# Kernel tuning notes

Measured on AMD Instinct MI355X. Metric: run time of the kernel, lower is better.

## Reference

```python
import jax, jax.numpy as jnp
import numpy as np

N, E, G = 20000, 640000, 64
D_IN, H, C, D_OUT = 256, 4, 64, 32
HC = H * C


def gat_layer(x, W, a_src, a_dst, b, src, dst, n_nodes, heads, ch):
    # x: [N, F_in], W: [F_in, H*C]
    h = (x @ W).reshape(n_nodes, heads, ch)          # [N,H,C]
    es = jnp.einsum('nhc,hc->nh', h, a_src)          # [N,H]
    ed = jnp.einsum('nhc,hc->nh', h, a_dst)
    e = jax.nn.leaky_relu(es[src] + ed[dst], 0.2)    # [Etot,H]
    m = jax.ops.segment_max(e, dst, num_segments=n_nodes)
    m = jnp.where(jnp.isfinite(m), m, 0.0)
    ex = jnp.exp(e - m[dst])
    denom = jax.ops.segment_sum(ex, dst, num_segments=n_nodes)
    alpha = ex / jnp.maximum(denom[dst], 1e-16)      # softmax over in-edges per dst
    out = jax.ops.segment_sum(alpha[:, :, None] * h[src], dst, num_segments=n_nodes)
    return out.reshape(n_nodes, heads * ch) + b


def setup_inputs() -> dict:
    key = jax.random.key(0)
    ks = jax.random.split(key, 14)
    g1 = 1.0 / np.sqrt(D_IN)
    g2 = 1.0 / np.sqrt(HC)
    inp = {
        'x': jax.random.normal(ks[0], (N, D_IN), jnp.float32),
        'edge_index': jax.random.randint(ks[1], (2, E), 0, N, jnp.int64 if jax.config.jax_enable_x64 else jnp.int32),
        'batch': jnp.sort(jax.random.randint(ks[2], (N,), 0, G)),
        'W1': jax.random.normal(ks[3], (D_IN, HC), jnp.float32) * g1,
        'a_src1': jax.random.normal(ks[4], (H, C), jnp.float32) * g2,
        'a_dst1': jax.random.normal(ks[5], (H, C), jnp.float32) * g2,
        'b1': jnp.zeros((HC,), jnp.float32),
        'W2': jax.random.normal(ks[6], (HC, HC), jnp.float32) * g2,
        'a_src2': jax.random.normal(ks[7], (H, C), jnp.float32) * g2,
        'a_dst2': jax.random.normal(ks[8], (H, C), jnp.float32) * g2,
        'b2': jnp.zeros((HC,), jnp.float32),
        'Wp': jax.random.normal(ks[9], (HC, D_OUT), jnp.float32) * g2,
        'bp': jnp.zeros((D_OUT,), jnp.float32),
    }
    return inp


def reference(x, edge_index, batch, W1, a_src1, a_dst1, b1, W2, a_src2, a_dst2, b2, Wp, bp):
    # add self-loops (PyG GATConv default)
    loop = jnp.arange(N, dtype=edge_index.dtype)
    src = jnp.concatenate([edge_index[0], loop])
    dst = jnp.concatenate([edge_index[1], loop])
    x1 = jax.nn.relu(gat_layer(x, W1, a_src1, a_dst1, b1, src, dst, N, H, C))
    # dropout p=0.6 is identity in eval mode
    x2 = jax.nn.relu(gat_layer(x1, W2, a_src2, a_dst2, b2, src, dst, N, H, C))
    node_scores = x2 @ Wp + bp                        # [N, D_OUT]
    sums = jax.ops.segment_sum(node_scores, batch, num_segments=G)
    counts = jax.ops.segment_sum(jnp.ones((N,), node_scores.dtype), batch, num_segments=G)
    return sums / jnp.maximum(counts, 1.0)[:, None]   # [G, D_OUT]
```

## Files before the change

kernel.cpp:

```cpp
#include <hip/hip_runtime.h>
#include <hip/hip_bf16.h>
#include <cstdint>

#define NNODES 20000
#define NEDGES 640000
#define ETOT   (NEDGES + NNODES)
#define NGROUP 64
#define HC     256
#define DOUT   32
#define EBLK   5120
#define NBLK   (NEDGES / EBLK)
#define CBLK   ((NNODES + 255) / 256)
#define GBLK   (NNODES / 16)
#define HALFN  10240

typedef short bf16x8 __attribute__((ext_vector_type(8)));
typedef short s16x4  __attribute__((ext_vector_type(4)));
typedef float f32x4  __attribute__((ext_vector_type(4)));
typedef float f32x2  __attribute__((ext_vector_type(2)));
typedef int   s32x4  __attribute__((ext_vector_type(4)));
typedef unsigned int u32x4 __attribute__((ext_vector_type(4)));

__device__ __forceinline__ float bs2f(short v) {
    union { unsigned int u; float f; } c; c.u = ((unsigned int)(unsigned short)v) << 16; return c.f;
}
__device__ __forceinline__ short f2bs(float v) {
    __hip_bfloat16 b = __float2bfloat16(v);
    union { __hip_bfloat16 b; short s; } u; u.b = b; return u.s;
}
__device__ __forceinline__ float ldf(const void* __restrict__ p, size_t i, int bf) {
    return bf ? __bfloat162float(((const __hip_bfloat16*)p)[i]) : ((const float*)p)[i];
}
__device__ __forceinline__ int ld_idx(const int* __restrict__ p, size_t i, int f64) {
    return f64 ? p[2 * i] : p[i];
}
__device__ __forceinline__ unsigned enc_f(float f) {
    unsigned u = __float_as_uint(f);
    return (u >> 31) ? ~u : (u | 0x80000000u);
}
__device__ __forceinline__ float dec_f(unsigned e) {
    return (e >> 31) ? __uint_as_float(e & 0x7FFFFFFFu) : __uint_as_float(~e);
}
__device__ __forceinline__ int probe_edge64(const int* __restrict__ ei) {
    int l = threadIdx.x & 63;
    int zeros = 0;
#pragma unroll
    for (int r = 0; r < 4; r++)
        zeros += __popcll(__ballot(ei[2 * (r * 64 + l) + 1] == 0));
    return (zeros > 200) ? 1 : 0;
}
__device__ __forceinline__ int probe_xbf(const unsigned int* __restrict__ xw) {
    int l = threadIdx.x & 63;
    int ones = 0;
#pragma unroll
    for (int r = 0; r < 4; r++)
        ones += __popcll(__ballot((xw[r * 64 + l] >> 14) & 1));
    return (ones < 64) ? 1 : 0;
}

__global__ __launch_bounds__(256) void k_setup(const unsigned int* __restrict__ xw,
                                               const int* __restrict__ ei,
                                               const int* __restrict__ bat,
                                               const void* __restrict__ W1, const void* __restrict__ W2,
                                               __hip_bfloat16* __restrict__ Wt1,
                                               __hip_bfloat16* __restrict__ Wt2,
                                               int* __restrict__ H,
                                               float* __restrict__ sx, int* __restrict__ cnt,
                                               unsigned* __restrict__ gp2) {
    __shared__ int hl[NNODES];
    int t = threadIdx.x, b = blockIdx.x;
    if (b < NBLK) {
        int f = probe_edge64(ei);
        s32x4* hl4 = reinterpret_cast<s32x4*>(hl);
        for (int i = t; i < NNODES / 4; i += 256) hl4[i] = (s32x4){0, 0, 0, 0};
        __syncthreads();
        int s0 = b * EBLK;
        if (f) {
            const int* d64 = ei + 2 * NEDGES;
            for (int i0 = s0; i0 < s0 + EBLK; i0 += 512) {
                int i = i0 + 2 * t;
                s32x4 v = *reinterpret_cast<const s32x4*>(d64 + 2 * (size_t)i);
                atomicAdd(&hl[v[0]], 1);
                atomicAdd(&hl[v[2]], 1);
            }
        } else {
            const int* d32 = ei + NEDGES;
            for (int i0 = s0; i0 < s0 + EBLK; i0 += 1024) {
                int i = i0 + 4 * t;
                s32x4 v = *reinterpret_cast<const s32x4*>(d32 + i);
                atomicAdd(&hl[v[0]], 1); atomicAdd(&hl[v[1]], 1);
                atomicAdd(&hl[v[2]], 1); atomicAdd(&hl[v[3]], 1);
            }
        }
        __syncthreads();
        s32x4* Hb4 = reinterpret_cast<s32x4*>(H + (size_t)b * NNODES);
        for (int i = t; i < NNODES / 4; i += 256) Hb4[i] = hl4[i];
    } else {
        int bf = probe_xbf(xw);
        int i = (b - NBLK) * 256 + t;
        int which = i >> 16;
        int j = i & 65535;
        int k = j >> 8, n = j & 255;
        const void* W = which ? W2 : W1;
        __hip_bfloat16* Wt = which ? Wt2 : Wt1;
        Wt[(size_t)n * 256 + k] = __float2bfloat16(ldf(W, (size_t)k * 256 + n, bf));
        if (b == NBLK) {
            for (int q = t; q < NGROUP * HC; q += 256) sx[q] = 0.f;
            if (t < 256) gp2[t] = 0x007FFFFFu;
            int f = probe_edge64(ei);
            if (t < NGROUP) hl[t] = 0;
            __syncthreads();
            for (int r = t; r < NNODES; r += 256) atomicAdd(&hl[ld_idx(bat, r, f)], 1);
            __syncthreads();
            if (t < NGROUP) cnt[t] = hl[t];
        }
    }
}

__global__ __launch_bounds__(256) void k_colsum(const int* __restrict__ H,
                                                int* __restrict__ deg,
                                                int* __restrict__ bsum) {
    __shared__ int wred[4];
    int t = threadIdx.x, n = blockIdx.x * 256 + t;
    int s = 0;
    if (n < NNODES) {
#pragma unroll 5
        for (int b = 0; b < NBLK; b++) s += H[(size_t)b * NNODES + n];
        s += 1;
        deg[n] = s;
    }
    int r = s;
#pragma unroll
    for (int o = 1; o < 64; o <<= 1) r += __shfl_xor(r, o);
    if ((t & 63) == 0) wred[t >> 6] = r;
    __syncthreads();
    if (t == 0) bsum[blockIdx.x] = wred[0] + wred[1] + wred[2] + wred[3];
}

__global__ __launch_bounds__(256) void k_base(int* __restrict__ H,
                                              const int* __restrict__ deg,
                                              const int* __restrict__ bsum,
                                              int* __restrict__ off,
                                              int* __restrict__ csr) {
    __shared__ int wtot[4];
    __shared__ int boff_s;
    int t = threadIdx.x, blk = blockIdx.x;
    int n = blk * 256 + t;
    int d = (n < NNODES) ? deg[n] : 0;
    int lane = t & 63, w = t >> 6;
    int sc = d;
#pragma unroll
    for (int o = 1; o < 64; o <<= 1) {
        int u = __shfl_up(sc, o);
        if (lane >= o) sc += u;
    }
    if (lane == 63) wtot[w] = sc;
    if (w == 0) {
        int v = (lane < blk) ? bsum[lane] : 0;
        if (lane + 64 < blk) v += bsum[lane + 64];
#pragma unroll
        for (int o = 1; o < 64; o <<= 1) v += __shfl_xor(v, o);
        if (lane == 0) boff_s = v;
    }
    __syncthreads();
    int woff = 0;
    for (int i = 0; i < w; i++) woff += wtot[i];
    int excl = woff + sc - d;
    if (blk == 0 && t == 0) off[NNODES] = ETOT;
    if (n < NNODES) {
        int o0 = boff_s + excl;
        off[n] = o0;
        csr[o0] = n;
        int run = o0 + 1;
#pragma unroll 5
        for (int b = 0; b < NBLK; b++) {
            size_t idx = (size_t)b * NNODES + n;
            int tt = H[idx];
            H[idx] = run;
            run += tt;
        }
    }
}

__device__ __forceinline__ void dev_scatter(int b, int f, const int* __restrict__ ei,
                                            const int* __restrict__ H, int* __restrict__ csr,
                                            int* hl) {
    int t = threadIdx.x;
    for (int pass = 0; pass < 2; ++pass) {
        int nbase = pass * HALFN;
        int span = NNODES - nbase; if (span > HALFN) span = HALFN;
        const int* Hb = H + (size_t)b * NNODES + nbase;
        for (int i = t; i < span; i += 256) hl[i] = Hb[i];
        __syncthreads();
        int s0 = b * EBLK;
        if (f) {
            const int* d64 = ei + 2 * NEDGES;
            for (int i0 = s0; i0 < s0 + EBLK; i0 += 512) {
                int i = i0 + 2 * t;
                s32x4 sv = *reinterpret_cast<const s32x4*>(ei + 2 * (size_t)i);
                s32x4 dv = *reinterpret_cast<const s32x4*>(d64 + 2 * (size_t)i);
                unsigned d0 = (unsigned)(dv[0] - nbase), d1 = (unsigned)(dv[2] - nbase);
                if (d0 < (unsigned)span) { int p = atomicAdd(&hl[d0], 1); csr[p] = sv[0]; }
                if (d1 < (unsigned)span) { int p = atomicAdd(&hl[d1], 1); csr[p] = sv[2]; }
            }
        } else {
            const int* d32 = ei + NEDGES;
            for (int i0 = s0; i0 < s0 + EBLK; i0 += 1024) {
                int i = i0 + 4 * t;
                s32x4 sv = *reinterpret_cast<const s32x4*>(ei + i);
                s32x4 dv = *reinterpret_cast<const s32x4*>(d32 + i);
#pragma unroll
                for (int k = 0; k < 4; k++) {
                    unsigned d = (unsigned)(dv[k] - nbase);
                    if (d < (unsigned)span) { int p = atomicAdd(&hl[d], 1); csr[p] = sv[k]; }
                }
            }
        }
        if (pass == 0) __syncthreads();
    }
}

__device__ __forceinline__ void dev_gemm(int tile, const void* __restrict__ A,
                                         const __hip_bfloat16* __restrict__ Bt,
                                         __hip_bfloat16* __restrict__ Hout,
                                         const void* __restrict__ a_src, const void* __restrict__ a_dst,
                                         float* __restrict__ es4, float* __restrict__ ed4,
                                         unsigned* __restrict__ gp2, int bf, int abf,
                                         u32x4* hst4) {
    int w    = threadIdx.x >> 6;
    int lane = threadIdx.x & 63;
    int mr   = lane & 15;
    int quad = lane >> 4;
    int r0   = tile * 16;
    f32x4 acc[4];
#pragma unroll
    for (int j = 0; j < 4; j++) acc[j] = (f32x4){0.f, 0.f, 0.f, 0.f};
    size_t rowoff = (size_t)(r0 + mr) * HC;
    const __hip_bfloat16* Btw = Bt + (size_t)w * 64 * HC;
    for (int kk = 0; kk < HC; kk += 32) {
        bf16x8 a;
        if (abf) {
            a = *reinterpret_cast<const bf16x8*>((const __hip_bfloat16*)A + rowoff + kk + quad * 8);
        } else {
            const float* af = (const float*)A + rowoff + kk + quad * 8;
            f32x4 lo = *reinterpret_cast<const f32x4*>(af);
            f32x4 hi = *reinterpret_cast<const f32x4*>(af + 4);
#pragma unroll
            for (int ii = 0; ii < 4; ii++) { a[ii] = f2bs(lo[ii]); a[ii + 4] = f2bs(hi[ii]); }
        }
#pragma unroll
        for (int j = 0; j < 4; j++) {
            bf16x8 b = *reinterpret_cast<const bf16x8*>(Btw + (size_t)(j * 16 + mr) * HC + kk + quad * 8);
            acc[j] = __builtin_amdgcn_mfma_f32_16x16x32_bf16(a, b, acc[j], 0, 0, 0);
        }
    }
    short* hst = reinterpret_cast<short*>(hst4);
#pragma unroll
    for (int j = 0; j < 4; j++)
#pragma unroll
        for (int r = 0; r < 4; r++)
            hst[(quad * 4 + r) * HC + w * 64 + j * 16 + mr] = f2bs(acc[j][r]);
    float ps[4] = {0.f, 0.f, 0.f, 0.f}, pd[4] = {0.f, 0.f, 0.f, 0.f};
#pragma unroll
    for (int j = 0; j < 4; j++) {
        float asv = ldf(a_src, (size_t)(w * 64 + j * 16 + mr), bf);
        float adv = ldf(a_dst, (size_t)(w * 64 + j * 16 + mr), bf);
#pragma unroll
        for (int r = 0; r < 4; r++) {
            ps[r] = fmaf(acc[j][r], asv, ps[r]);
            pd[r] = fmaf(acc[j][r], adv, pd[r]);
        }
    }
#pragma unroll
    for (int o = 1; o < 16; o <<= 1)
#pragma unroll
        for (int r = 0; r < 4; r++) {
            ps[r] += __shfl_xor(ps[r], o);
            pd[r] += __shfl_xor(pd[r], o);
        }
    float pm = fmaxf(fmaxf(ps[0], ps[1]), fmaxf(ps[2], ps[3]));
    pm = fmaxf(pm, __shfl_xor(pm, 16));
    pm = fmaxf(pm, __shfl_xor(pm, 32));
    if (lane == 0) atomicMax(&gp2[w * 64 + (tile & 63)], enc_f(pm));
    if (mr == 0)
#pragma unroll
        for (int r = 0; r < 4; r++) {
            int row = r0 + quad * 4 + r;
            es4[(size_t)row * 4 + w] = ps[r];
            ed4[(size_t)row * 4 + w] = pd[r];
        }
    __syncthreads();
    u32x4* dst = reinterpret_cast<u32x4*>((short*)Hout + (size_t)r0 * HC);
    dst[threadIdx.x]       = hst4[threadIdx.x];
    dst[threadIdx.x + 256] = hst4[threadIdx.x + 256];
}

__global__ __launch_bounds__(256) void k_sg1(const void* __restrict__ x,
                                             const int* __restrict__ ei,
                                             const int* __restrict__ H, int* __restrict__ csr,
                                             const __hip_bfloat16* __restrict__ Wt1,
                                             __hip_bfloat16* __restrict__ hb,
                                             const void* __restrict__ as1, const void* __restrict__ ad1,
                                             float* __restrict__ es, float* __restrict__ ed,
                                             unsigned* __restrict__ gp2) {
    __shared__ int smem[HALFN];
    int b = blockIdx.x;
    if (b < NBLK) {
        int f = probe_edge64(ei);
        dev_scatter(b, f, ei, H, csr, smem);
    } else {
        int bf = probe_xbf((const unsigned int*)x);
        dev_gemm(b - NBLK, x, Wt1, hb, as1, ad1, es, ed, gp2, bf, bf, (u32x4*)smem);
    }
}

__global__ __launch_bounds__(256) void k_gemm2(const void* __restrict__ x,
                                               const __hip_bfloat16* __restrict__ xb,
                                               const __hip_bfloat16* __restrict__ Wt2,
                                               __hip_bfloat16* __restrict__ hb,
                                               const void* __restrict__ as2, const void* __restrict__ ad2,
                                               float* __restrict__ es, float* __restrict__ ed,
                                               unsigned* __restrict__ gp2) {
    __shared__ u32x4 hst4[512];
    int bf = probe_xbf((const unsigned int*)x);
    dev_gemm(blockIdx.x, xb, Wt2, hb, as2, ad2, es, ed, gp2, bf, 1, hst4);
}

__global__ __launch_bounds__(256) void k_agg(const void* __restrict__ x,
                                             const __hip_bfloat16* __restrict__ Hb,
                                             const float* __restrict__ es4, const float* __restrict__ ed4,
                                             const void* __restrict__ bias,
                                             const int* __restrict__ off, const int* __restrict__ csr,
                                             const unsigned* __restrict__ gp2,
                                             __hip_bfloat16* __restrict__ out) {
    __shared__ float p_lds[4][4][64];
    __shared__ int   s_lds[4][64];
    __shared__ float gm_s[4];
    int wv = threadIdx.x >> 6;
    int l  = threadIdx.x & 63;
    int half = l >> 5;
    int hl   = l & 31;
    int hd8  = hl >> 3;
    int bf = probe_xbf((const unsigned int*)x);
    {
        float m = dec_f(gp2[wv * 64 + l]);
#pragma unroll
        for (int o = 32; o; o >>= 1) m = fmaxf(m, __shfl_xor(m, o));
        if (l == 0) gm_s[wv] = m;
    }
    __syncthreads();
    f32x4 gm = (f32x4){gm_s[0], gm_s[1], gm_s[2], gm_s[3]};
    int n0 = blockIdx.x * 4 + wv;
    for (int n = n0; n < NNODES; n += 10000) {
        int base = off[n], deg = off[n + 1] - base;
        f32x4 edv = *reinterpret_cast<const f32x4*>(ed4 + (size_t)n * 4);
        f32x4 M;
#pragma unroll
        for (int h = 0; h < 4; h++) {
            float t0 = gm[h] + edv[h];
            M[h] = (t0 > 0.f) ? t0 : 0.2f * t0;
        }
        f32x4 dsum = (f32x4){0.f, 0.f, 0.f, 0.f};
        f32x2 acc2[4];
#pragma unroll
        for (int d = 0; d < 4; d++) acc2[d] = (f32x2){0.f, 0.f};
        for (int c0 = 0; c0 < deg; c0 += 64) {
            int cn = min(deg - c0, 64);
            int s = 0;
            f32x4 pv = (f32x4){0.f, 0.f, 0.f, 0.f};
            if (l < cn) {
                s = csr[base + c0 + l];
                f32x4 e = *reinterpret_cast<const f32x4*>(es4 + (size_t)s * 4);
#pragma unroll
                for (int h = 0; h < 4; h++) {
                    float t = e[h] + edv[h];
                    t = (t > 0.f) ? t : 0.2f * t;
                    pv[h] = __expf(t - M[h]);
                }
            }
            s_lds[wv][l] = s;
#pragma unroll
            for (int h = 0; h < 4; h++) p_lds[wv][h][l] = pv[h];
#pragma unroll
            for (int h = 0; h < 4; h++) dsum[h] += pv[h];
            int jn = (cn + 15) & ~15;
            for (int j = 0; j < jn; j += 16) {
                int e0 = j + 8 * half;
                s32x4 sA = *reinterpret_cast<const s32x4*>(&s_lds[wv][e0]);
                s32x4 sB = *reinterpret_cast<const s32x4*>(&s_lds[wv][e0 + 4]);
                f32x4 pA = *reinterpret_cast<const f32x4*>(&p_lds[wv][hd8][e0]);
                f32x4 pB = *reinterpret_cast<const f32x4*>(&p_lds[wv][hd8][e0 + 4]);
                u32x4 hv[8];
#pragma unroll
                for (int i = 0; i < 8; i++) {
                    int sj = (i < 4) ? sA[i & 3] : sB[i & 3];
                    hv[i] = *reinterpret_cast<const u32x4*>(Hb + (size_t)sj * HC + hl * 8);
                }
#pragma unroll
                for (int i = 0; i < 8; i++) {
                    float p = (i < 4) ? pA[i & 3] : pB[i & 3];
#pragma unroll
                    for (int d = 0; d < 4; d++) {
                        unsigned int u = hv[i][d];
                        f32x2 h2;
                        h2.x = __uint_as_float(u << 16);
                        h2.y = __uint_as_float(u & 0xFFFF0000u);
                        acc2[d] += h2 * p;
                    }
                }
            }
        }
#pragma unroll
        for (int o = 32; o; o >>= 1)
#pragma unroll
            for (int h = 0; h < 4; h++) dsum[h] += __shfl_xor(dsum[h], o);
#pragma unroll
        for (int d = 0; d < 4; d++) {
            acc2[d].x += __shfl_xor(acc2[d].x, 32);
            acc2[d].y += __shfl_xor(acc2[d].y, 32);
        }
        float rinv = 1.0f / fmaxf(dsum[hd8], 1e-16f);
        if (half == 0) {
            bf16x8 ov;
#pragma unroll
            for (int d = 0; d < 4; d++) {
                float v0 = acc2[d].x * rinv + ldf(bias, (size_t)hl * 8 + 2 * d, bf);
                float v1 = acc2[d].y * rinv + ldf(bias, (size_t)hl * 8 + 2 * d + 1, bf);
                ov[2 * d]     = f2bs(fmaxf(v0, 0.f));
                ov[2 * d + 1] = f2bs(fmaxf(v1, 0.f));
            }
            *reinterpret_cast<bf16x8*>(out + (size_t)n * HC + hl * 8) = ov;
        }
    }
}

__global__ __launch_bounds__(256) void k_groupsum(const int* __restrict__ ei,
                                                  const __hip_bfloat16* __restrict__ X2,
                                                  const int* __restrict__ batch,
                                                  float* __restrict__ sx) {
    const int RPB = NNODES / 250;
    int b = blockIdx.x;
    int f = probe_edge64(ei);
    int sub = threadIdx.x >> 6, l = threadIdx.x & 63;
    int r = b * RPB + sub;
    f32x4 acc = (f32x4){0.f, 0.f, 0.f, 0.f};
    int curg = ld_idx(batch, r, f);
    for (int k = 0; k < RPB / 4; k++, r += 4) {
        int g = ld_idx(batch, r, f);
        if (g != curg) {
#pragma unroll
            for (int c = 0; c < 4; c++) atomicAdd(&sx[(size_t)curg * HC + l * 4 + c], acc[c]);
            acc = (f32x4){0.f, 0.f, 0.f, 0.f}; curg = g;
        }
        s16x4 hv = *reinterpret_cast<const s16x4*>(X2 + (size_t)r * HC + l * 4);
#pragma unroll
        for (int c = 0; c < 4; c++) acc[c] += bs2f(hv[c]);
    }
#pragma unroll
    for (int c = 0; c < 4; c++) atomicAdd(&sx[(size_t)curg * HC + l * 4 + c], acc[c]);
}

__global__ __launch_bounds__(256) void k_final(const void* __restrict__ x,
                                               const float* __restrict__ sx,
                                               const void* __restrict__ Wp,
                                               const void* __restrict__ bp,
                                               const int* __restrict__ cnt,
                                               void* __restrict__ out) {
    __shared__ float red[8][32];
    int g = blockIdx.x, t = threadIdx.x;
    int c = t & 31, seg = t >> 5;
    int bf = probe_xbf((const unsigned int*)x);
    const float* sxg = sx + (size_t)g * HC;
    float a = 0.f;
#pragma unroll
    for (int k = 0; k < 32; k++) {
        int kk = seg * 32 + k;
        a = fmaf(sxg[kk], ldf(Wp, (size_t)kk * DOUT + c, bf), a);
    }
    red[seg][c] = a;
    __syncthreads();
    if (t < 32) {
        float s = 0.f;
#pragma unroll
        for (int i = 0; i < 8; i++) s += red[i][t];
        int ct = cnt[g];
        float v = (ct > 0) ? (s / ct + ldf(bp, (size_t)t, bf)) : 0.f;
        if (bf) ((__hip_bfloat16*)out)[g * DOUT + t] = __float2bfloat16(v);
        else    ((float*)out)[g * DOUT + t]          = v;
    }
}

extern "C" void kernel_launch(void* const* d_in, const int* in_sizes, int n_in,
                              void* d_out, int out_size, void* d_ws, size_t ws_size,
                              hipStream_t stream) {
    (void)in_sizes; (void)n_in; (void)out_size; (void)ws_size;
    const void* x   = d_in[0];
    const int*  ei  = (const int*)d_in[1];
    const int*  bat = (const int*)d_in[2];
    const void* W1  = d_in[3];
    const void* as1 = d_in[4];
    const void* ad1 = d_in[5];
    const void* b1  = d_in[6];
    const void* W2  = d_in[7];
    const void* as2 = d_in[8];
    const void* ad2 = d_in[9];
    const void* b2  = d_in[10];
    const void* Wp  = d_in[11];
    const void* bp  = d_in[12];

    char* ws = (char*)d_ws;
    size_t o = 0;
    auto alloc = [&](size_t bytes) -> char* {
        char* p = ws + o;
        o += (bytes + 255) & ~(size_t)255;
        return p;
    };
    __hip_bfloat16* hb  = (__hip_bfloat16*)alloc((size_t)NNODES * HC * 2);
    __hip_bfloat16* xb  = (__hip_bfloat16*)alloc((size_t)NNODES * HC * 2);
    __hip_bfloat16* xb2 = (__hip_bfloat16*)alloc((size_t)NNODES * HC * 2);
    __hip_bfloat16* Wt1 = (__hip_bfloat16*)alloc((size_t)HC * HC * 2);
    __hip_bfloat16* Wt2 = (__hip_bfloat16*)alloc((size_t)HC * HC * 2);
    float* es = (float*)alloc((size_t)NNODES * 4 * 4);
    float* ed = (float*)alloc((size_t)NNODES * 4 * 4);
    int* H    = (int*)alloc((size_t)NBLK * NNODES * 4);
    int* deg  = (int*)alloc((size_t)NNODES * 4);
    int* off  = (int*)alloc((size_t)(NNODES + 1) * 4);
    int* csr  = (int*)alloc((size_t)ETOT * 4);
    int* bsum = (int*)alloc((size_t)CBLK * 4);
    unsigned* gp2 = (unsigned*)alloc(256 * 4);
    float* sx = (float*)alloc((size_t)NGROUP * HC * 4);
    int* cnt  = (int*)alloc(256);

    k_setup<<<NBLK + 512, 256, 0, stream>>>((const unsigned int*)x, ei, bat, W1, W2,
                                            Wt1, Wt2, H, sx, cnt, gp2);
    k_colsum<<<CBLK, 256, 0, stream>>>(H, deg, bsum);
    k_base<<<CBLK, 256, 0, stream>>>(H, deg, bsum, off, csr);
    k_sg1<<<NBLK + GBLK, 256, 0, stream>>>(x, ei, H, csr, Wt1, hb, as1, ad1, es, ed, gp2);
    k_agg<<<2500, 256, 0, stream>>>(x, hb, es, ed, b1, off, csr, gp2, xb);
    k_gemm2<<<GBLK, 256, 0, stream>>>(x, xb, Wt2, hb, as2, ad2, es, ed, gp2);
    k_agg<<<2500, 256, 0, stream>>>(x, hb, es, ed, b2, off, csr, gp2, xb2);
    k_groupsum<<<250, 256, 0, stream>>>(ei, xb2, bat, sx);
    k_final<<<NGROUP, 256, 0, stream>>>(x, sx, Wp, bp, cnt, d_out);
}
```

Measured before the change: 300.4 us.

## Merge pipeline stages into fewer kernels using in-kernel atomic counter barriers

Collapses the nine launches into four by fusing colsum/base/scatter/gemm1, agg1/gemm2 and agg2/groupsum/final into single kernels. Consumer blocks spin on global atomic counters that producer blocks bump after a threadfence. The CSR scatter now does global atomics directly on H instead of staging each half in LDS. This is meant to remove launch gaps and tail idle time between stages. It relies on producer blocks being scheduled before spinning consumers, which risks deadlock or serialization. The global atomics may also cost more than the LDS version did.

```diff
diff --git a/kernel.cpp b/kernel.cpp
--- a/kernel.cpp
+++ b/kernel.cpp
@@ -9,10 +9,11 @@
 #define HC     256
 #define DOUT   32
 #define EBLK   5120
-#define NBLK   (NEDGES / EBLK)
-#define CBLK   ((NNODES + 255) / 256)
-#define GBLK   (NNODES / 16)
-#define HALFN  10240
+#define NBLK   125
+#define CBLK   79
+#define GBLK   1250
+#define G2BLK  625
+#define ABLK   2500
 
 typedef short bf16x8 __attribute__((ext_vector_type(8)));
 typedef short s16x4  __attribute__((ext_vector_type(4)));
@@ -56,6 +57,19 @@
     for (int r = 0; r < 4; r++)
         ones += __popcll(__ballot((xw[r * 64 + l] >> 14) & 1));
     return (ones < 64) ? 1 : 0;
+}
+__device__ __forceinline__ void signal_done(int* ctr) {
+    __threadfence();
+    __syncthreads();
+    if (threadIdx.x == 0) atomicAdd(ctr, 1);
+}
+__device__ __forceinline__ void spin_wait(int* ctr, int target) {
+    if (threadIdx.x == 0) {
+        while (__hip_atomic_load(ctr, __ATOMIC_RELAXED, __HIP_MEMORY_SCOPE_AGENT) < target)
+            __builtin_amdgcn_s_sleep(8);
+    }
+    __syncthreads();
+    __threadfence();
 }
 
 __global__ __launch_bounds__(256) void k_setup(const unsigned int* __restrict__ xw,
@@ -66,7 +80,7 @@
                                                __hip_bfloat16* __restrict__ Wt2,
                                                int* __restrict__ H,
                                                float* __restrict__ sx, int* __restrict__ cnt,
-                                               unsigned* __restrict__ gp2) {
+                                               unsigned* __restrict__ gp2, int* __restrict__ sy) {
     __shared__ int hl[NNODES];
     int t = threadIdx.x, b = blockIdx.x;
     if (b < NBLK) {
@@ -107,6 +121,7 @@
         if (b == NBLK) {
             for (int q = t; q < NGROUP * HC; q += 256) sx[q] = 0.f;
             if (t < 256) gp2[t] = 0x007FFFFFu;
+            if (t < 8) sy[t] = 0;
             int f = probe_edge64(ei);
             if (t < NGROUP) hl[t] = 0;
             __syncthreads();
@@ -114,109 +129,6 @@
             __syncthreads();
             if (t < NGROUP) cnt[t] = hl[t];
         }
-    }
-}
-
-__global__ __launch_bounds__(256) void k_colsum(const int* __restrict__ H,
-                                                int* __restrict__ deg,
-                                                int* __restrict__ bsum) {
-    __shared__ int wred[4];
-    int t = threadIdx.x, n = blockIdx.x * 256 + t;
-    int s = 0;
-    if (n < NNODES) {
-#pragma unroll 5
-        for (int b = 0; b < NBLK; b++) s += H[(size_t)b * NNODES + n];
-        s += 1;
-        deg[n] = s;
-    }
-    int r = s;
-#pragma unroll
-    for (int o = 1; o < 64; o <<= 1) r += __shfl_xor(r, o);
-    if ((t & 63) == 0) wred[t >> 6] = r;
-    __syncthreads();
-    if (t == 0) bsum[blockIdx.x] = wred[0] + wred[1] + wred[2] + wred[3];
-}
-
-__global__ __launch_bounds__(256) void k_base(int* __restrict__ H,
-                                              const int* __restrict__ deg,
-                                              const int* __restrict__ bsum,
-                                              int* __restrict__ off,
-                                              int* __restrict__ csr) {
-    __shared__ int wtot[4];
-    __shared__ int boff_s;
-    int t = threadIdx.x, blk = blockIdx.x;
-    int n = blk * 256 + t;
-    int d = (n < NNODES) ? deg[n] : 0;
-    int lane = t & 63, w = t >> 6;
-    int sc = d;
-#pragma unroll
-    for (int o = 1; o < 64; o <<= 1) {
-        int u = __shfl_up(sc, o);
-        if (lane >= o) sc += u;
-    }
-    if (lane == 63) wtot[w] = sc;
-    if (w == 0) {
-        int v = (lane < blk) ? bsum[lane] : 0;
-        if (lane + 64 < blk) v += bsum[lane + 64];
-#pragma unroll
-        for (int o = 1; o < 64; o <<= 1) v += __shfl_xor(v, o);
-        if (lane == 0) boff_s = v;
-    }
-    __syncthreads();
-    int woff = 0;
-    for (int i = 0; i < w; i++) woff += wtot[i];
-    int excl = woff + sc - d;
-    if (blk == 0 && t == 0) off[NNODES] = ETOT;
-    if (n < NNODES) {
-        int o0 = boff_s + excl;
-        off[n] = o0;
-        csr[o0] = n;
-        int run = o0 + 1;
-#pragma unroll 5
-        for (int b = 0; b < NBLK; b++) {
-            size_t idx = (size_t)b * NNODES + n;
-            int tt = H[idx];
-            H[idx] = run;
-            run += tt;
-        }
-    }
-}
-
-__device__ __forceinline__ void dev_scatter(int b, int f, const int* __restrict__ ei,
-                                            const int* __restrict__ H, int* __restrict__ csr,
-                                            int* hl) {
-    int t = threadIdx.x;
-    for (int pass = 0; pass < 2; ++pass) {
-        int nbase = pass * HALFN;
-        int span = NNODES - nbase; if (span > HALFN) span = HALFN;
-        const int* Hb = H + (size_t)b * NNODES + nbase;
-        for (int i = t; i < span; i += 256) hl[i] = Hb[i];
-        __syncthreads();
-        int s0 = b * EBLK;
-        if (f) {
-            const int* d64 = ei + 2 * NEDGES;
-            for (int i0 = s0; i0 < s0 + EBLK; i0 += 512) {
-                int i = i0 + 2 * t;
-                s32x4 sv = *reinterpret_cast<const s32x4*>(ei + 2 * (size_t)i);
-                s32x4 dv = *reinterpret_cast<const s32x4*>(d64 + 2 * (size_t)i);
-                unsigned d0 = (unsigned)(dv[0] - nbase), d1 = (unsigned)(dv[2] - nbase);
-                if (d0 < (unsigned)span) { int p = atomicAdd(&hl[d0], 1); csr[p] = sv[0]; }
-                if (d1 < (unsigned)span) { int p = atomicAdd(&hl[d1], 1); csr[p] = sv[2]; }
-            }
-        } else {
-            const int* d32 = ei + NEDGES;
-            for (int i0 = s0; i0 < s0 + EBLK; i0 += 1024) {
-                int i = i0 + 4 * t;
-                s32x4 sv = *reinterpret_cast<const s32x4*>(ei + i);
-                s32x4 dv = *reinterpret_cast<const s32x4*>(d32 + i);
-#pragma unroll
-                for (int k = 0; k < 4; k++) {
-                    unsigned d = (unsigned)(dv[k] - nbase);
-                    if (d < (unsigned)span) { int p = atomicAdd(&hl[d], 1); csr[p] = sv[k]; }
-                }
-            }
-        }
-        if (pass == 0) __syncthreads();
     }
 }
 
@@ -293,55 +205,118 @@
     u32x4* dst = reinterpret_cast<u32x4*>((short*)Hout + (size_t)r0 * HC);
     dst[threadIdx.x]       = hst4[threadIdx.x];
     dst[threadIdx.x + 256] = hst4[threadIdx.x + 256];
-}
-
-__global__ __launch_bounds__(256) void k_sg1(const void* __restrict__ x,
-                                             const int* __restrict__ ei,
-                                             const int* __restrict__ H, int* __restrict__ csr,
-                                             const __hip_bfloat16* __restrict__ Wt1,
-                                             __hip_bfloat16* __restrict__ hb,
-                                             const void* __restrict__ as1, const void* __restrict__ ad1,
-                                             float* __restrict__ es, float* __restrict__ ed,
-                                             unsigned* __restrict__ gp2) {
-    __shared__ int smem[HALFN];
-    int b = blockIdx.x;
-    if (b < NBLK) {
+    __syncthreads();
+}
+
+__global__ __launch_bounds__(256) void k_p2(const void* __restrict__ x,
+                                            const int* __restrict__ ei,
+                                            int* __restrict__ H, int* __restrict__ bsum,
+                                            int* __restrict__ off, int* __restrict__ csr,
+                                            const __hip_bfloat16* __restrict__ Wt1,
+                                            __hip_bfloat16* __restrict__ hb,
+                                            const void* __restrict__ as1, const void* __restrict__ ad1,
+                                            float* __restrict__ es, float* __restrict__ ed,
+                                            unsigned* __restrict__ gp2, int* __restrict__ sy) {
+    __shared__ int smem[2048];
+    int bid = blockIdx.x, t = threadIdx.x;
+    if (bid < CBLK) {
+        int n = bid * 256 + t;
+        int lane = t & 63, w = t >> 6;
+        int d = 0;
+        if (n < NNODES) {
+#pragma unroll 5
+            for (int b = 0; b < NBLK; b++) d += H[(size_t)b * NNODES + n];
+            d += 1;
+        }
+        int r = d;
+#pragma unroll
+        for (int o = 1; o < 64; o <<= 1) r += __shfl_xor(r, o);
+        if (lane == 0) smem[w] = r;
+        __syncthreads();
+        if (t == 0) bsum[bid] = smem[0] + smem[1] + smem[2] + smem[3];
+        signal_done(&sy[0]);
+        spin_wait(&sy[0], CBLK);
+        int sc = d;
+#pragma unroll
+        for (int o = 1; o < 64; o <<= 1) {
+            int u = __shfl_up(sc, o);
+            if (lane >= o) sc += u;
+        }
+        if (lane == 63) smem[w] = sc;
+        if (w == 0) {
+            int v = (lane < bid) ? bsum[lane] : 0;
+            if (lane + 64 < bid) v += bsum[lane + 64];
+#pragma unroll
+            for (int o = 1; o < 64; o <<= 1) v += __shfl_xor(v, o);
+            if (lane == 0) smem[4] = v;
+        }
+        __syncthreads();
+        int woff = 0;
+        for (int i = 0; i < w; i++) woff += smem[i];
+        int excl = woff + sc - d;
+        if (bid == 0 && t == 0) off[NNODES] = ETOT;
+        if (n < NNODES) {
+            int o0 = smem[4] + excl;
+            off[n] = o0;
+            csr[o0] = n;
+            int run = o0 + 1;
+#pragma unroll 5
+            for (int b = 0; b < NBLK; b++) {
+                size_t idx = (size_t)b * NNODES + n;
+                int tt = H[idx];
+                H[idx] = run;
+                run += tt;
+            }
+        }
+        signal_done(&sy[1]);
+    } else if (bid < CBLK + NBLK) {
+        int b = bid - CBLK;
         int f = probe_edge64(ei);
-        dev_scatter(b, f, ei, H, csr, smem);
+        spin_wait(&sy[1], CBLK);
+        int* Hb = H + (size_t)b * NNODES;
+        int s0 = b * EBLK;
+        if (f) {
+            const int* d64 = ei + 2 * NEDGES;
+            for (int i0 = s0; i0 < s0 + EBLK; i0 += 512) {
+                int i = i0 + 2 * t;
+                s32x4 sv = *reinterpret_cast<const s32x4*>(ei + 2 * (size_t)i);
+                s32x4 dv = *reinterpret_cast<const s32x4*>(d64 + 2 * (size_t)i);
+                int p0 = atomicAdd(&Hb[dv[0]], 1); csr[p0] = sv[0];
+                int p1 = atomicAdd(&Hb[dv[2]], 1); csr[p1] = sv[2];
+            }
+        } else {
+            const int* d32 = ei + NEDGES;
+            for (int i0 = s0; i0 < s0 + EBLK; i0 += 1024) {
+                int i = i0 + 4 * t;
+                s32x4 sv = *reinterpret_cast<const s32x4*>(ei + i);
+                s32x4 dv = *reinterpret_cast<const s32x4*>(d32 + i);
+#pragma unroll
+                for (int k = 0; k < 4; k++) {
+                    int p = atomicAdd(&Hb[dv[k]], 1); csr[p] = sv[k];
+                }
+            }
+        }
     } else {
         int bf = probe_xbf((const unsigned int*)x);
-        dev_gemm(b - NBLK, x, Wt1, hb, as1, ad1, es, ed, gp2, bf, bf, (u32x4*)smem);
-    }
-}
-
-__global__ __launch_bounds__(256) void k_gemm2(const void* __restrict__ x,
-                                               const __hip_bfloat16* __restrict__ xb,
-                                               const __hip_bfloat16* __restrict__ Wt2,
-                                               __hip_bfloat16* __restrict__ hb,
-                                               const void* __restrict__ as2, const void* __restrict__ ad2,
-                                               float* __restrict__ es, float* __restrict__ ed,
-                                               unsigned* __restrict__ gp2) {
-    __shared__ u32x4 hst4[512];
-    int bf = probe_xbf((const unsigned int*)x);
-    dev_gemm(blockIdx.x, xb, Wt2, hb, as2, ad2, es, ed, gp2, bf, 1, hst4);
-}
-
-__global__ __launch_bounds__(256) void k_agg(const void* __restrict__ x,
-                                             const __hip_bfloat16* __restrict__ Hb,
-                                             const float* __restrict__ es4, const float* __restrict__ ed4,
-                                             const void* __restrict__ bias,
-                                             const int* __restrict__ off, const int* __restrict__ csr,
-                                             const unsigned* __restrict__ gp2,
-                                             __hip_bfloat16* __restrict__ out) {
-    __shared__ float p_lds[4][4][64];
-    __shared__ int   s_lds[4][64];
-    __shared__ float gm_s[4];
+        dev_gemm(bid - (CBLK + NBLK), x, Wt1, hb, as1, ad1, es, ed, gp2, bf, bf,
+                 (u32x4*)smem);
+    }
+}
+
+__device__ __forceinline__ void dev_agg(int nb0, const __hip_bfloat16* __restrict__ Hb,
+                                        const float* __restrict__ es4, const float* __restrict__ ed4,
+                                        const void* __restrict__ bias,
+                                        const int* __restrict__ off, const int* __restrict__ csr,
+                                        const unsigned* __restrict__ gp2, int bf,
+                                        __hip_bfloat16* __restrict__ out, int* smem) {
     int wv = threadIdx.x >> 6;
     int l  = threadIdx.x & 63;
     int half = l >> 5;
     int hl   = l & 31;
     int hd8  = hl >> 3;
-    int bf = probe_xbf((const unsigned int*)x);
+    float* pw = (float*)smem + wv * 256;
+    int*   sw = smem + 1024 + wv * 64;
+    float* gm_s = (float*)(smem + 1280);
     {
         float m = dec_f(gp2[wv * 64 + l]);
 #pragma unroll
@@ -350,8 +325,7 @@
     }
     __syncthreads();
     f32x4 gm = (f32x4){gm_s[0], gm_s[1], gm_s[2], gm_s[3]};
-    int n0 = blockIdx.x * 4 + wv;
-    for (int n = n0; n < NNODES; n += 10000) {
+    for (int n = nb0 + wv; n < NNODES; n += 10000) {
         int base = off[n], deg = off[n + 1] - base;
         f32x4 edv = *reinterpret_cast<const f32x4*>(ed4 + (size_t)n * 4);
         f32x4 M;
@@ -378,18 +352,18 @@
                     pv[h] = __expf(t - M[h]);
                 }
             }
-            s_lds[wv][l] = s;
-#pragma unroll
-            for (int h = 0; h < 4; h++) p_lds[wv][h][l] = pv[h];
+            sw[l] = s;
+#pragma unroll
+            for (int h = 0; h < 4; h++) pw[h * 64 + l] = pv[h];
 #pragma unroll
             for (int h = 0; h < 4; h++) dsum[h] += pv[h];
             int jn = (cn + 15) & ~15;
             for (int j = 0; j < jn; j += 16) {
                 int e0 = j + 8 * half;
-                s32x4 sA = *reinterpret_cast<const s32x4*>(&s_lds[wv][e0]);
-                s32x4 sB = *reinterpret_cast<const s32x4*>(&s_lds[wv][e0 + 4]);
-                f32x4 pA = *reinterpret_cast<const f32x4*>(&p_lds[wv][hd8][e0]);
-                f32x4 pB = *reinterpret_cast<const f32x4*>(&p_lds[wv][hd8][e0 + 4]);
+                s32x4 sA = *reinterpret_cast<const s32x4*>(&sw[e0]);
+                s32x4 sB = *reinterpret_cast<const s32x4*>(&sw[e0 + 4]);
+                f32x4 pA = *reinterpret_cast<const f32x4*>(&pw[hd8 * 64 + e0]);
+                f32x4 pB = *reinterpret_cast<const f32x4*>(&pw[hd8 * 64 + e0 + 4]);
                 u32x4 hv[8];
 #pragma unroll
                 for (int i = 0; i < 8; i++) {
@@ -434,59 +408,97 @@
     }
 }
 
-__global__ __launch_bounds__(256) void k_groupsum(const int* __restrict__ ei,
-                                                  const __hip_bfloat16* __restrict__ X2,
-                                                  const int* __restrict__ batch,
-                                                  float* __restrict__ sx) {
-    const int RPB = NNODES / 250;
-    int b = blockIdx.x;
-    int f = probe_edge64(ei);
-    int sub = threadIdx.x >> 6, l = threadIdx.x & 63;
-    int r = b * RPB + sub;
-    f32x4 acc = (f32x4){0.f, 0.f, 0.f, 0.f};
-    int curg = ld_idx(batch, r, f);
-    for (int k = 0; k < RPB / 4; k++, r += 4) {
-        int g = ld_idx(batch, r, f);
-        if (g != curg) {
-#pragma unroll
-            for (int c = 0; c < 4; c++) atomicAdd(&sx[(size_t)curg * HC + l * 4 + c], acc[c]);
-            acc = (f32x4){0.f, 0.f, 0.f, 0.f}; curg = g;
-        }
-        s16x4 hv = *reinterpret_cast<const s16x4*>(X2 + (size_t)r * HC + l * 4);
-#pragma unroll
-        for (int c = 0; c < 4; c++) acc[c] += bs2f(hv[c]);
-    }
-#pragma unroll
-    for (int c = 0; c < 4; c++) atomicAdd(&sx[(size_t)curg * HC + l * 4 + c], acc[c]);
-}
-
-__global__ __launch_bounds__(256) void k_final(const void* __restrict__ x,
-                                               const float* __restrict__ sx,
-                                               const void* __restrict__ Wp,
-                                               const void* __restrict__ bp,
-                                               const int* __restrict__ cnt,
-                                               void* __restrict__ out) {
-    __shared__ float red[8][32];
-    int g = blockIdx.x, t = threadIdx.x;
-    int c = t & 31, seg = t >> 5;
+__global__ __launch_bounds__(256) void k_p3(const void* __restrict__ x,
+                                            const __hip_bfloat16* __restrict__ hb,
+                                            __hip_bfloat16* __restrict__ hb_mut,
+                                            const float* __restrict__ es, const float* __restrict__ ed,
+                                            float* __restrict__ es_mut, float* __restrict__ ed_mut,
+                                            const void* __restrict__ b1,
+                                            const int* __restrict__ off, const int* __restrict__ csr,
+                                            unsigned* __restrict__ gp2,
+                                            __hip_bfloat16* __restrict__ xb,
+                                            const __hip_bfloat16* __restrict__ Wt2,
+                                            const void* __restrict__ as2, const void* __restrict__ ad2,
+                                            int* __restrict__ sy) {
+    __shared__ int smem[2048];
+    int bid = blockIdx.x;
     int bf = probe_xbf((const unsigned int*)x);
-    const float* sxg = sx + (size_t)g * HC;
-    float a = 0.f;
-#pragma unroll
-    for (int k = 0; k < 32; k++) {
-        int kk = seg * 32 + k;
-        a = fmaf(sxg[kk], ldf(Wp, (size_t)kk * DOUT + c, bf), a);
-    }
-    red[seg][c] = a;
-    __syncthreads();
-    if (t < 32) {
-        float s = 0.f;
-#pragma unroll
-        for (int i = 0; i < 8; i++) s += red[i][t];
-        int ct = cnt[g];
-        float v = (ct > 0) ? (s / ct + ldf(bp, (size_t)t, bf)) : 0.f;
-        if (bf) ((__hip_bfloat16*)out)[g * DOUT + t] = __float2bfloat16(v);
-        else    ((float*)out)[g * DOUT + t]          = v;
+    if (bid < ABLK) {
+        dev_agg(bid * 4, hb, es, ed, b1, off, csr, gp2, bf, xb, smem);
+        signal_done(&sy[2]);
+    } else {
+        spin_wait(&sy[2], ABLK);
+        int t0 = bid - ABLK;
+        dev_gemm(t0, xb, Wt2, hb_mut, as2, ad2, es_mut, ed_mut, gp2, bf, 1, (u32x4*)smem);
+        dev_gemm(t0 + G2BLK, xb, Wt2, hb_mut, as2, ad2, es_mut, ed_mut, gp2, bf, 1, (u32x4*)smem);
+    }
+}
+
+__global__ __launch_bounds__(256) void k_p4(const void* __restrict__ x,
+                                            const int* __restrict__ ei,
+                                            const __hip_bfloat16* __restrict__ hb,
+                                            const float* __restrict__ es, const float* __restrict__ ed,
+                                            const void* __restrict__ b2,
+                                            const int* __restrict__ off, const int* __restrict__ csr,
+                                            const unsigned* __restrict__ gp2,
+                                            __hip_bfloat16* __restrict__ xb2,
+                                            const int* __restrict__ bat,
+                                            float* __restrict__ sx, const int* __restrict__ cnt,
+                                            const void* __restrict__ Wp, const void* __restrict__ bp,
+                                            void* __restrict__ out, int* __restrict__ sy) {
+    __shared__ int smem[2048];
+    int bid = blockIdx.x, t = threadIdx.x;
+    if (bid < ABLK) {
+        int bf = probe_xbf((const unsigned int*)x);
+        dev_agg(bid * 4, hb, es, ed, b2, off, csr, gp2, bf, xb2, smem);
+        signal_done(&sy[3]);
+    } else if (bid < ABLK + 250) {
+        int f = probe_edge64(ei);
+        spin_wait(&sy[3], ABLK);
+        const int RPB = NNODES / 250;
+        int b = bid - ABLK;
+        int sub = t >> 6, l = t & 63;
+        int r = b * RPB + sub;
+        f32x4 acc = (f32x4){0.f, 0.f, 0.f, 0.f};
+        int curg = ld_idx(bat, r, f);
+        for (int k = 0; k < RPB / 4; k++, r += 4) {
+            int g = ld_idx(bat, r, f);
+            if (g != curg) {
+#pragma unroll
+                for (int c = 0; c < 4; c++) atomicAdd(&sx[(size_t)curg * HC + l * 4 + c], acc[c]);
+                acc = (f32x4){0.f, 0.f, 0.f, 0.f}; curg = g;
+            }
+            s16x4 hv = *reinterpret_cast<const s16x4*>(xb2 + (size_t)r * HC + l * 4);
+#pragma unroll
+            for (int c = 0; c < 4; c++) acc[c] += bs2f(hv[c]);
+        }
+#pragma unroll
+        for (int c = 0; c < 4; c++) atomicAdd(&sx[(size_t)curg * HC + l * 4 + c], acc[c]);
+        signal_done(&sy[4]);
+    } else {
+        int bf = probe_xbf((const unsigned int*)x);
+        spin_wait(&sy[4], 250);
+        float* red = (float*)smem;
+        int g = bid - (ABLK + 250);
+        int c = t & 31, seg = t >> 5;
+        const float* sxg = sx + (size_t)g * HC;
+        float a = 0.f;
+#pragma unroll
+        for (int k = 0; k < 32; k++) {
+            int kk = seg * 32 + k;
+            a = fmaf(sxg[kk], ldf(Wp, (size_t)kk * DOUT + c, bf), a);
+        }
+        red[seg * 32 + c] = a;
+        __syncthreads();
+        if (t < 32) {
+            float s = 0.f;
+#pragma unroll
+            for (int i = 0; i < 8; i++) s += red[i * 32 + t];
+            int ct = cnt[g];
+            float v = (ct > 0) ? (s / ct + ldf(bp, (size_t)t, bf)) : 0.f;
+            if (bf) ((__hip_bfloat16*)out)[g * DOUT + t] = __float2bfloat16(v);
+            else    ((float*)out)[g * DOUT + t]          = v;
+        }
     }
 }
 
@@ -523,22 +535,21 @@
     float* es = (float*)alloc((size_t)NNODES * 4 * 4);
     float* ed = (float*)alloc((size_t)NNODES * 4 * 4);
     int* H    = (int*)alloc((size_t)NBLK * NNODES * 4);
-    int* deg  = (int*)alloc((size_t)NNODES * 4);
     int* off  = (int*)alloc((size_t)(NNODES + 1) * 4);
     int* csr  = (int*)alloc((size_t)ETOT * 4);
     int* bsum = (int*)alloc((size_t)CBLK * 4);
     unsigned* gp2 = (unsigned*)alloc(256 * 4);
     float* sx = (float*)alloc((size_t)NGROUP * HC * 4);
     int* cnt  = (int*)alloc(256);
+    int* sy   = (int*)alloc(256);
 
     k_setup<<<NBLK + 512, 256, 0, stream>>>((const unsigned int*)x, ei, bat, W1, W2,
-                                            Wt1, Wt2, H, sx, cnt, gp2);
-    k_colsum<<<CBLK, 256, 0, stream>>>(H, deg, bsum);
-    k_base<<<CBLK, 256, 0, stream>>>(H, deg, bsum, off, csr);
-    k_sg1<<<NBLK + GBLK, 256, 0, stream>>>(x, ei, H, csr, Wt1, hb, as1, ad1, es, ed, gp2);
-    k_agg<<<2500, 256, 0, stream>>>(x, hb, es, ed, b1, off, csr, gp2, xb);
-    k_gemm2<<<GBLK, 256, 0, stream>>>(x, xb, Wt2, hb, as2, ad2, es, ed, gp2);
-    k_agg<<<2500, 256, 0, stream>>>(x, hb, es, ed, b2, off, csr, gp2, xb2);
-    k_groupsum<<<250, 256, 0, stream>>>(ei, xb2, bat, sx);
-    k_final<<<NGROUP, 256, 0, stream>>>(x, sx, Wp, bp, cnt, d_out);
-}
+                                            Wt1, Wt2, H, sx, cnt, gp2, sy);
+    k_p2<<<CBLK + NBLK + GBLK, 256, 0, stream>>>(x, ei, H, bsum, off, csr, Wt1, hb,
+                                                 as1, ad1, es, ed, gp2, sy);
+    k_p3<<<ABLK + G2BLK, 256, 0, stream>>>(x, hb, hb, es, ed, es, ed, b1, off, csr,
+                                           gp2, xb, Wt2, as2, ad2, sy);
+    k_p4<<<ABLK + 250 + NGROUP, 256, 0, stream>>>(x, ei, hb, es, ed, b2, off, csr,
+                                                  gp2, xb2, bat, sx, cnt, Wp, bp,
+                                                  d_out, sy);
+}
```

Result: slower. 1.120 ms (+272.7%).
